# Kernel optimization log

Hardware: AMD Instinct MI355X
Metric: run time of the kernel (lower is better)

Reference implementation:

```python
import jax, jax.numpy as jnp
import numpy as np

KH, KW = 3, 3      # kernel_size
FILTERS = 32
MINVAL, MAXVAL = -0.45, -0.15


def setup_inputs() -> dict:
    key = jax.random.key(0)
    k1, k2 = jax.random.split(key)
    x = jax.random.normal(k1, (16, 256, 256, 1), dtype=jnp.float32)
    # dilation_weights: (1, 1, 1, kh*kw, filters), RandomUniform(minval, maxval)
    w = jax.random.uniform(k2, (1, 1, 1, KH * KW, FILTERS),
                           minval=MINVAL, maxval=MAXVAL, dtype=jnp.float32)
    return {"x": x, "w": w}


def reference(x, w):
    # x: (B, H, W, 1) channels_last; w: (1, 1, 1, kh*kw, filters)
    B, H, W, _ = x.shape
    Ho, Wo = H - KH + 1, W - KW + 1  # VALID padding, stride 1
    # extract_patches equivalent: (B, Ho, Wo, kh*kw), row-major over window
    patches = jnp.stack(
        [x[:, i:i + Ho, j:j + Wo, 0] for i in range(KH) for j in range(KW)],
        axis=-1,
    )
    # broadcast-add structuring element, max-reduce over patch dim (tropical conv)
    return jnp.max(patches[..., None] + w, axis=3)  # (B, Ho, Wo, filters)
```

## Files before the change

kernel.cpp:

```cpp
#include <hip/hip_runtime.h>


#define BB 16
#define HH 256
#define WW 256
#define KHH 3
#define KWW 3
#define FF 32
#define HO (HH - KHH + 1)
#define WO (WW - KWW + 1)

__global__ __launch_bounds__(256) void
dilate_kernel(const float* __restrict__ x, const float* __restrict__ w,
              float* __restrict__ out) {
    const long long tid = (long long)blockIdx.x * blockDim.x + threadIdx.x;
    const int fq  = (int)(tid & 7);
    const long long pix = tid >> 3;
    if (pix >= (long long)BB * HO * WO) return;

    const int j = (int)(pix % WO);
    const int t = (int)(pix / WO);
    const int i = t % HO;
    const int b = t / HO;

    const float* xb = x + ((long long)b * HH + i) * WW + j;
    float xv[9];
#pragma unroll
    for (int di = 0; di < 3; ++di) {
#pragma unroll
        for (int dj = 0; dj < 3; ++dj) {
            xv[di * 3 + dj] = xb[di * WW + dj];
        }
    }

    const float4* __restrict__ w4 = (const float4*)w;

    float4 wv = w4[fq];
    float4 m;
    m.x = xv[0] + wv.x;
    m.y = xv[0] + wv.y;
    m.z = xv[0] + wv.z;
    m.w = xv[0] + wv.w;
#pragma unroll
    for (int p = 1; p < 9; ++p) {
        wv = w4[p * 8 + fq];
        m.x = fmaxf(m.x, xv[p] + wv.x);
        m.y = fmaxf(m.y, xv[p] + wv.y);
        m.z = fmaxf(m.z, xv[p] + wv.z);
        m.w = fmaxf(m.w, xv[p] + wv.w);
    }

    ((float4*)out)[pix * 8 + fq] = m;
}

extern "C" void kernel_launch(void* const* d_in, const int* in_sizes, int n_in,
                              void* d_out, int out_size, void* d_ws, size_t ws_size,
                              hipStream_t stream) {
    const float* x = (const float*)d_in[0];
    const float* w = (const float*)d_in[1];
    float* out = (float*)d_out;

    const long long total_threads = (long long)BB * HO * WO * 8;
    const int block = 256;
    const int grid = (int)((total_threads + block - 1) / block);

    dilate_kernel<<<grid, block, 0, stream>>>(x, w, out);
}
```

Baseline: 171.6 us.

## Compute two adjacent pixels per thread with 3D grid and vector loads

Each thread now handles two horizontally adjacent output pixels for its four filters. It loads a 3x4 input window with float2 loads, which shares input loads across the two pixels and hoists all nine weight vectors into registers. A 3D grid (column tiles, rows, batch) replaces the 64-bit divide/modulo index math. This halves the thread count and removes the per-thread index arithmetic, at the cost of more registers and idle threads in the last column tile per row.

```diff
diff --git a/kernel.cpp b/kernel.cpp
--- a/kernel.cpp
+++ b/kernel.cpp
@@ -4,53 +4,63 @@
 #define BB 16
 #define HH 256
 #define WW 256
-#define KHH 3
-#define KWW 3
 #define FF 32
-#define HO (HH - KHH + 1)
-#define WO (WW - KWW + 1)
+#define HO 254
+#define WO 254
 
 __global__ __launch_bounds__(256) void
 dilate_kernel(const float* __restrict__ x, const float* __restrict__ w,
               float* __restrict__ out) {
-    const long long tid = (long long)blockIdx.x * blockDim.x + threadIdx.x;
-    const int fq  = (int)(tid & 7);
-    const long long pix = tid >> 3;
-    if (pix >= (long long)BB * HO * WO) return;
+    const int fq = threadIdx.x & 7;
+    const int pp = threadIdx.x >> 3;
+    const int j0 = (blockIdx.x << 6) + (pp << 1);
+    if (j0 >= WO) return;
+    const int i = blockIdx.y;
+    const int b = blockIdx.z;
 
-    const int j = (int)(pix % WO);
-    const int t = (int)(pix / WO);
-    const int i = t % HO;
-    const int b = t / HO;
+    const float4* __restrict__ w4 = (const float4*)w + fq;
+    float4 wv[9];
+#pragma unroll
+    for (int p = 0; p < 9; ++p) wv[p] = w4[p * 8];
 
-    const float* xb = x + ((long long)b * HH + i) * WW + j;
-    float xv[9];
+    const float* xb = x + ((b * HH + i) * WW + j0);
+    float xv[3][4];
 #pragma unroll
-    for (int di = 0; di < 3; ++di) {
+    for (int r = 0; r < 3; ++r) {
+        const float2 lo = *(const float2*)(xb + r * WW);
+        const float2 hi = *(const float2*)(xb + r * WW + 2);
+        xv[r][0] = lo.x; xv[r][1] = lo.y; xv[r][2] = hi.x; xv[r][3] = hi.y;
+    }
+
+    float4 m0, m1;
 #pragma unroll
-        for (int dj = 0; dj < 3; ++dj) {
-            xv[di * 3 + dj] = xb[di * WW + dj];
+    for (int r = 0; r < 3; ++r) {
+#pragma unroll
+        for (int c = 0; c < 3; ++c) {
+            const int p = r * 3 + c;
+            const float a0 = xv[r][c];
+            const float a1 = xv[r][c + 1];
+            if (p == 0) {
+                m0.x = a0 + wv[0].x; m0.y = a0 + wv[0].y;
+                m0.z = a0 + wv[0].z; m0.w = a0 + wv[0].w;
+                m1.x = a1 + wv[0].x; m1.y = a1 + wv[0].y;
+                m1.z = a1 + wv[0].z; m1.w = a1 + wv[0].w;
+            } else {
+                m0.x = fmaxf(m0.x, a0 + wv[p].x);
+                m0.y = fmaxf(m0.y, a0 + wv[p].y);
+                m0.z = fmaxf(m0.z, a0 + wv[p].z);
+                m0.w = fmaxf(m0.w, a0 + wv[p].w);
+                m1.x = fmaxf(m1.x, a1 + wv[p].x);
+                m1.y = fmaxf(m1.y, a1 + wv[p].y);
+                m1.z = fmaxf(m1.z, a1 + wv[p].z);
+                m1.w = fmaxf(m1.w, a1 + wv[p].w);
+            }
         }
     }
 
-    const float4* __restrict__ w4 = (const float4*)w;
-
-    float4 wv = w4[fq];
-    float4 m;
-    m.x = xv[0] + wv.x;
-    m.y = xv[0] + wv.y;
-    m.z = xv[0] + wv.z;
-    m.w = xv[0] + wv.w;
-#pragma unroll
-    for (int p = 1; p < 9; ++p) {
-        wv = w4[p * 8 + fq];
-        m.x = fmaxf(m.x, xv[p] + wv.x);
-        m.y = fmaxf(m.y, xv[p] + wv.y);
-        m.z = fmaxf(m.z, xv[p] + wv.z);
-        m.w = fmaxf(m.w, xv[p] + wv.w);
-    }
-
-    ((float4*)out)[pix * 8 + fq] = m;
+    float4* o4 = (float4*)out + (((b * HO + i) * WO + j0) * 8 + fq);
+    o4[0] = m0;
+    o4[8] = m1;
 }
 
 extern "C" void kernel_launch(void* const* d_in, const int* in_sizes, int n_in,
@@ -60,9 +70,6 @@
     const float* w = (const float*)d_in[1];
     float* out = (float*)d_out;
 
-    const long long total_threads = (long long)BB * HO * WO * 8;
-    const int block = 256;
-    const int grid = (int)((total_threads + block - 1) / block);
-
-    dilate_kernel<<<grid, block, 0, stream>>>(x, w, out);
+    dim3 grid((WO + 63) / 64, HO, BB);
+    dilate_kernel<<<grid, 256, 0, stream>>>(x, w, out);
 }
```

Result: faster. 157.7 us (-8.1%).
